# Optimization experiments

Hardware: AMD Instinct MI355X
Metric: run time of the kernel (lower is better)

Reference implementation:

```python
import jax, jax.numpy as jnp
import numpy as np
import math

B, S, D, H = 4, 1024, 1024, 16
DK = D // H
WINDOW = 128
NEG = -100000.0


def setup_inputs() -> dict:
    key = jax.random.key(0)
    kx, kw1, kb1, kw2, kb2 = jax.random.split(key, 5)
    x = jax.random.normal(kx, (B, S, D), dtype=jnp.float32)
    # sliding-window band mask: True where |i-j| <= WINDOW
    i = jnp.arange(S)
    band = (jnp.abs(i[:, None] - i[None, :]) <= WINDOW)
    mask = jnp.broadcast_to(band, (B, S, S))
    # second structured mask: causal
    causal = (i[:, None] >= i[None, :])
    mask2 = jnp.broadcast_to(causal, (B, S, S))
    scale = 1.0 / math.sqrt(D)
    Wqkv = jax.random.normal(kw1, (D, 3 * D), dtype=jnp.float32) * scale
    bqkv = jax.random.normal(kb1, (3 * D,), dtype=jnp.float32) * 0.01
    Wo = jax.random.normal(kw2, (D, D), dtype=jnp.float32) * scale
    bo = jax.random.normal(kb2, (D,), dtype=jnp.float32) * 0.01
    return {"x": x, "mask": mask, "mask2": mask2, "Wqkv": Wqkv, "bqkv": bqkv, "Wo": Wo, "bo": bo}


def reference(x, mask, mask2, Wqkv, bqkv, Wo, bo):
    b, s, d = x.shape
    qkv = x @ Wqkv + bqkv                      # [b, s, 3d]
    q, k, v = jnp.split(qkv, 3, axis=-1)
    # [b, s, h, dk] -> [b, h, s, dk]
    q = q.reshape(b, s, H, DK).transpose(0, 2, 1, 3)
    k = k.reshape(b, s, H, DK).transpose(0, 2, 1, 3)
    v = v.reshape(b, s, H, DK).transpose(0, 2, 1, 3)
    scores = jnp.einsum('bhtd,bhsd->bhts', q, k) / math.sqrt(DK)
    scores = jnp.where(mask[:, None, :, :], scores, NEG)
    scores = jnp.where(mask2[:, None, :, :], scores, NEG)
    weights = jax.nn.softmax(scores, axis=-1)  # [b, h, t, s]
    context = jnp.einsum('bhts,bhsd->bhtd', weights, v)
    context = context.transpose(0, 2, 1, 3).reshape(b, s, d)
    context = context @ Wo + bo
    return (context, weights)
```

## Files before the change

kernel.cpp:

```cpp
#include <hip/hip_runtime.h>

typedef short bf16x8 __attribute__((ext_vector_type(8)));
typedef float floatx4 __attribute__((ext_vector_type(4)));

#define GLOBAL_AS __attribute__((address_space(1)))
#define LDS_AS __attribute__((address_space(3)))

__device__ __forceinline__ void gload_lds16(const ushort* g, ushort* l) {
  __builtin_amdgcn_global_load_lds((const GLOBAL_AS void*)g, (LDS_AS void*)l, 16, 0, 0);
}

__device__ __forceinline__ ushort f2bf(float x) {
  uint u = __float_as_uint(x);
  return (ushort)((u + 0x7fffu + ((u >> 16) & 1u)) >> 16);
}

__global__ __launch_bounds__(256) void k_f32_to_bf16(const float4* __restrict__ in,
                                                     ushort4* __restrict__ out, int n4) {
  int g = blockIdx.x * 256 + threadIdx.x;
  if (g < n4) {
    float4 v = in[g];
    ushort4 o;
    o.x = f2bf(v.x); o.y = f2bf(v.y); o.z = f2bf(v.z); o.w = f2bf(v.w);
    out[g] = o;
  }
}

__global__ __launch_bounds__(256) void k_transpose2(const float* __restrict__ W1,
                                                    ushort* __restrict__ O1,
                                                    const float* __restrict__ W2,
                                                    ushort* __restrict__ O2) {
  __shared__ float tile[32][33];
  int bx = blockIdx.x;
  const float* in; ushort* out; int N;
  if (bx < 96) { in = W1; out = O1; N = 3072; }
  else         { in = W2; out = O2; N = 1024; bx -= 96; }
  const int K = 1024;
  int n0 = bx * 32, k0 = blockIdx.y * 32;
  int tx = threadIdx.x & 31, ty = threadIdx.x >> 5;
  #pragma unroll
  for (int r = ty; r < 32; r += 8)
    tile[r][tx] = in[(size_t)(k0 + r) * N + n0 + tx];
  __syncthreads();
  #pragma unroll
  for (int r = ty; r < 32; r += 8)
    out[(size_t)(n0 + r) * K + k0 + tx] = f2bf(tile[tx][r]);
}

template <int OUT_BF16, int BN>
__global__ __launch_bounds__(256) void k_gemm_bt(const ushort* __restrict__ A,
                                                 const ushort* __restrict__ Bt,
                                                 const float* __restrict__ bias,
                                                 void* __restrict__ Cout,
                                                 int M, int N, int K) {
  constexpr int NI = BN / 32;
  constexpr int NB = BN / 64;
  __shared__ ushort As[128 * 32];
  __shared__ ushort Bs[BN * 32];
  const int t = threadIdx.x;
  const int m0 = blockIdx.y * 128, n0 = blockIdx.x * BN;
  const int w = t >> 6, l = t & 63;
  const int wm = (w & 1) * 64, wn = (w >> 1) * (BN / 2);
  const int lr = l & 15, q8 = (l >> 4) * 8;
  const int lrow = l >> 2, lcol = (l & 3) * 8;

  floatx4 acc[4][NI];
  #pragma unroll
  for (int i = 0; i < 4; ++i)
    #pragma unroll
    for (int j = 0; j < NI; ++j) acc[i][j] = (floatx4){0.f, 0.f, 0.f, 0.f};

  for (int k0 = 0; k0 < K; k0 += 32) {
    __syncthreads();
    #pragma unroll
    for (int i = 0; i < 2; ++i) {
      int r0 = (w * 2 + i) * 16;
      gload_lds16(A + (size_t)(m0 + r0 + lrow) * K + k0 + lcol, As + r0 * 32);
    }
    #pragma unroll
    for (int i = 0; i < NB; ++i) {
      int r0 = (w * NB + i) * 16;
      gload_lds16(Bt + (size_t)(n0 + r0 + lrow) * K + k0 + lcol, Bs + r0 * 32);
    }
    __syncthreads();
    bf16x8 af[4], bfr[NI];
    #pragma unroll
    for (int mi = 0; mi < 4; ++mi)
      af[mi] = *(const bf16x8*)(As + (wm + mi * 16 + lr) * 32 + q8);
    #pragma unroll
    for (int ni = 0; ni < NI; ++ni)
      bfr[ni] = *(const bf16x8*)(Bs + (wn + ni * 16 + lr) * 32 + q8);
    #pragma unroll
    for (int mi = 0; mi < 4; ++mi)
      #pragma unroll
      for (int ni = 0; ni < NI; ++ni)
        acc[mi][ni] = __builtin_amdgcn_mfma_f32_16x16x32_bf16(af[mi], bfr[ni], acc[mi][ni], 0, 0, 0);
  }

  const int rq = (l >> 4) * 4;
  #pragma unroll
  for (int ni = 0; ni < NI; ++ni) {
    int col = n0 + wn + ni * 16 + lr;
    float bv = bias[col];
    #pragma unroll
    for (int mi = 0; mi < 4; ++mi) {
      int row = m0 + wm + mi * 16 + rq;
      #pragma unroll
      for (int r2 = 0; r2 < 4; ++r2) {
        float v = acc[mi][ni][r2] + bv;
        size_t idx = (size_t)(row + r2) * N + col;
        if (OUT_BF16) ((ushort*)Cout)[idx] = f2bf(v);
        else          ((float*)Cout)[idx] = v;
      }
    }
  }
}

__global__ __launch_bounds__(256) void k_attn(const ushort* __restrict__ qkv,
                                              float* __restrict__ wout,
                                              ushort* __restrict__ ctxout) {
  __shared__ ushort smKP[192 * 68];
  __shared__ ushort smVT[64 * 202];
  __shared__ ushort smQ[64 * 68];

  const int t = threadIdx.x;
  const int w = t >> 6, l = t & 63;
  const int lr = l & 15, q8 = (l >> 4) * 8, q4 = (l >> 4) * 4;
  const int iblk = blockIdx.x & 15;
  const int h = (blockIdx.x >> 4) & 15;
  const int b = blockIdx.x >> 8;
  const int i0 = iblk * 64;
  const int jb0 = i0 - 128;
  const int tok0 = b * 1024 + i0;
  const int qoff = h * 64, koff = 1024 + h * 64, voff = 2048 + h * 64;
  const size_t wbase = ((size_t)(b * 16 + h) * 1024 + i0) * 1024;

  {
    int jstart = jb0 < 0 ? 0 : jb0;
    int jend = i0 + 64;
    float4 z = {0.f, 0.f, 0.f, 0.f};
    for (int g = t; g < 64 * 256; g += 256) {
      int r = g >> 8, j = (g & 255) * 4;
      if (j < jstart || j >= jend)
        *(float4*)(wout + wbase + (size_t)r * 1024 + j) = z;
    }
  }

  #pragma unroll
  for (int c = 0; c < 2; ++c) {
    int idx = t + 256 * c, row = idx >> 3, ch = idx & 7;
    *(uint4*)(smQ + row * 68 + ch * 8) =
        *(const uint4*)(qkv + (size_t)(tok0 + row) * 3072 + qoff + ch * 8);
  }
  #pragma unroll
  for (int c = 0; c < 6; ++c) {
    int idx = t + 256 * c, row = idx >> 3, ch = idx & 7;
    int jsrc = jb0 + row; if (jsrc < 0) jsrc = 0;
    *(uint4*)(smKP + row * 68 + ch * 8) =
        *(const uint4*)(qkv + (size_t)(b * 1024 + jsrc) * 3072 + koff + ch * 8);
  }
  #pragma unroll
  for (int c = 0; c < 6; ++c) {
    int idx = t + 256 * c;
    int j = (idx & 15) + 16 * (idx >> 7);
    int d0 = ((idx >> 4) & 7) * 8;
    int jsrc = jb0 + j; if (jsrc < 0) jsrc = 0;
    uint4 u = *(const uint4*)(qkv + (size_t)(b * 1024 + jsrc) * 3072 + voff + d0);
    ushort* p = smVT + j;
    p[(d0 + 0) * 202] = (ushort)(u.x & 0xffffu);
    p[(d0 + 1) * 202] = (ushort)(u.x >> 16);
    p[(d0 + 2) * 202] = (ushort)(u.y & 0xffffu);
    p[(d0 + 3) * 202] = (ushort)(u.y >> 16);
    p[(d0 + 4) * 202] = (ushort)(u.z & 0xffffu);
    p[(d0 + 5) * 202] = (ushort)(u.z >> 16);
    p[(d0 + 6) * 202] = (ushort)(u.w & 0xffffu);
    p[(d0 + 7) * 202] = (ushort)(u.w >> 16);
  }
  __syncthreads();

  floatx4 sc[12];
  #pragma unroll
  for (int ni = 0; ni < 12; ++ni) sc[ni] = (floatx4){0.f, 0.f, 0.f, 0.f};
  bf16x8 aq0 = *(const bf16x8*)(smQ + (w * 16 + lr) * 68 + q8);
  bf16x8 aq1 = *(const bf16x8*)(smQ + (w * 16 + lr) * 68 + 32 + q8);
  #pragma unroll
  for (int ni = 0; ni < 12; ++ni) {
    bf16x8 bk0 = *(const bf16x8*)(smKP + (ni * 16 + lr) * 68 + q8);
    bf16x8 bk1 = *(const bf16x8*)(smKP + (ni * 16 + lr) * 68 + 32 + q8);
    sc[ni] = __builtin_amdgcn_mfma_f32_16x16x32_bf16(aq0, bk0, sc[ni], 0, 0, 0);
    sc[ni] = __builtin_amdgcn_mfma_f32_16x16x32_bf16(aq1, bk1, sc[ni], 0, 0, 0);
  }
  __syncthreads();

  float mrow[4] = {-3e38f, -3e38f, -3e38f, -3e38f};
  #pragma unroll
  for (int ni = 0; ni < 12; ++ni) {
    int nj = ni * 16 + lr;
    #pragma unroll
    for (int reg = 0; reg < 4; ++reg) {
      int di = w * 16 + q4 + reg;
      bool valid = (nj >= di) & (nj <= di + 128) & (jb0 + nj >= 0);
      float s = valid ? sc[ni][reg] * 0.125f : -3e38f;
      sc[ni][reg] = s;
      mrow[reg] = fmaxf(mrow[reg], s);
    }
  }
  #pragma unroll
  for (int reg = 0; reg < 4; ++reg) {
    #pragma unroll
    for (int off = 1; off < 16; off <<= 1)
      mrow[reg] = fmaxf(mrow[reg], __shfl_xor(mrow[reg], off, 64));
  }
  float lrow[4] = {0.f, 0.f, 0.f, 0.f};
  #pragma unroll
  for (int ni = 0; ni < 12; ++ni) {
    #pragma unroll
    for (int reg = 0; reg < 4; ++reg) {
      float e = __expf(sc[ni][reg] - mrow[reg]);
      sc[ni][reg] = e;
      lrow[reg] += e;
    }
  }
  float inv[4];
  #pragma unroll
  for (int reg = 0; reg < 4; ++reg) {
    float s = lrow[reg];
    #pragma unroll
    for (int off = 1; off < 16; off <<= 1) s += __shfl_xor(s, off, 64);
    inv[reg] = 1.0f / s;
  }

  ushort* smP = smKP;
  #pragma unroll
  for (int ni = 0; ni < 12; ++ni) {
    int nj = ni * 16 + lr;
    int j = jb0 + nj;
    #pragma unroll
    for (int reg = 0; reg < 4; ++reg) {
      int il = w * 16 + q4 + reg;
      float e = sc[ni][reg];
      if (j >= 0) wout[wbase + (size_t)il * 1024 + j] = e * inv[reg];
      smP[il * 202 + nj] = f2bf(e);
    }
  }

  floatx4 oc[4];
  #pragma unroll
  for (int ni = 0; ni < 4; ++ni) oc[ni] = (floatx4){0.f, 0.f, 0.f, 0.f};
  #pragma unroll
  for (int ks = 0; ks < 6; ++ks) {
    bf16x8 ap = *(const bf16x8*)(smP + (w * 16 + lr) * 202 + ks * 32 + q8);
    #pragma unroll
    for (int ni = 0; ni < 4; ++ni) {
      bf16x8 bv = *(const bf16x8*)(smVT + (ni * 16 + lr) * 202 + ks * 32 + q8);
      oc[ni] = __builtin_amdgcn_mfma_f32_16x16x32_bf16(ap, bv, oc[ni], 0, 0, 0);
    }
  }

  #pragma unroll
  for (int ni = 0; ni < 4; ++ni) {
    int d = ni * 16 + lr;
    #pragma unroll
    for (int reg = 0; reg < 4; ++reg) {
      int il = w * 16 + q4 + reg;
      ctxout[(size_t)(tok0 + il) * 1024 + qoff + d] = f2bf(oc[ni][reg] * inv[reg]);
    }
  }
}

extern "C" void kernel_launch(void* const* d_in, const int* in_sizes, int n_in,
                              void* d_out, int out_size, void* d_ws, size_t ws_size,
                              hipStream_t stream) {
  const float* x    = (const float*)d_in[0];
  const float* Wqkv = (const float*)d_in[3];
  const float* bqkv = (const float*)d_in[4];
  const float* Wo   = (const float*)d_in[5];
  const float* bo   = (const float*)d_in[6];

  float* out_ctx = (float*)d_out;
  float* out_w   = out_ctx + (size_t)4 * 1024 * 1024;

  char* ws = (char*)d_ws;
  ushort* qkv_bf = (ushort*)(ws);
  ushort* ctx_bf = (ushort*)(ws + 25165824);
  ushort* x_bf   = (ushort*)(ws + 33554432);
  ushort* WqkvT  = (ushort*)(ws + 41943040);
  ushort* WoT    = (ushort*)(ws + 48234496);

  k_f32_to_bf16<<<4096, 256, 0, stream>>>((const float4*)x, (ushort4*)x_bf, 1048576);
  k_transpose2<<<dim3(128, 32), 256, 0, stream>>>(Wqkv, WqkvT, Wo, WoT);
  k_gemm_bt<1, 128><<<dim3(24, 32), 256, 0, stream>>>(x_bf, WqkvT, bqkv, qkv_bf, 4096, 3072, 1024);
  k_attn<<<1024, 256, 0, stream>>>(qkv_bf, out_w, ctx_bf);
  k_gemm_bt<0, 64><<<dim3(16, 32), 256, 0, stream>>>(ctx_bf, WoT, bo, out_ctx, 4096, 1024, 1024);
}
```

Measured before the change: 407.5 us.

## Write attention weights in one coalesced full-row pass from LDS

The separate zero-fill pass and the scattered per-element weight stores are replaced by a final pass. After the PV matmul, each thread writes a float4 column slice of all 64 rows with nontemporal stores, reading the probabilities from the bf16 P tile in LDS and scaling by per-row inverse sums kept in shared memory. This aims to make the large weights write fully coalesced and to write each output byte only once. Q is now loaded straight from global memory into registers instead of being staged in LDS, and the LDS strides are adjusted. The trade-off is that the weights output now comes from bf16-rounded exponentials rather than fp32 values, which lowers its accuracy.

```diff
diff --git a/kernel.cpp b/kernel.cpp
--- a/kernel.cpp
+++ b/kernel.cpp
@@ -120,8 +120,8 @@
                                               float* __restrict__ wout,
                                               ushort* __restrict__ ctxout) {
   __shared__ ushort smKP[192 * 68];
-  __shared__ ushort smVT[64 * 202];
-  __shared__ ushort smQ[64 * 68];
+  __shared__ ushort smVT[64 * 200];
+  __shared__ float smInv[64];
 
   const int t = threadIdx.x;
   const int w = t >> 6, l = t & 63;
@@ -135,23 +135,6 @@
   const int qoff = h * 64, koff = 1024 + h * 64, voff = 2048 + h * 64;
   const size_t wbase = ((size_t)(b * 16 + h) * 1024 + i0) * 1024;
 
-  {
-    int jstart = jb0 < 0 ? 0 : jb0;
-    int jend = i0 + 64;
-    float4 z = {0.f, 0.f, 0.f, 0.f};
-    for (int g = t; g < 64 * 256; g += 256) {
-      int r = g >> 8, j = (g & 255) * 4;
-      if (j < jstart || j >= jend)
-        *(float4*)(wout + wbase + (size_t)r * 1024 + j) = z;
-    }
-  }
-
-  #pragma unroll
-  for (int c = 0; c < 2; ++c) {
-    int idx = t + 256 * c, row = idx >> 3, ch = idx & 7;
-    *(uint4*)(smQ + row * 68 + ch * 8) =
-        *(const uint4*)(qkv + (size_t)(tok0 + row) * 3072 + qoff + ch * 8);
-  }
   #pragma unroll
   for (int c = 0; c < 6; ++c) {
     int idx = t + 256 * c, row = idx >> 3, ch = idx & 7;
@@ -167,22 +150,24 @@
     int jsrc = jb0 + j; if (jsrc < 0) jsrc = 0;
     uint4 u = *(const uint4*)(qkv + (size_t)(b * 1024 + jsrc) * 3072 + voff + d0);
     ushort* p = smVT + j;
-    p[(d0 + 0) * 202] = (ushort)(u.x & 0xffffu);
-    p[(d0 + 1) * 202] = (ushort)(u.x >> 16);
-    p[(d0 + 2) * 202] = (ushort)(u.y & 0xffffu);
-    p[(d0 + 3) * 202] = (ushort)(u.y >> 16);
-    p[(d0 + 4) * 202] = (ushort)(u.z & 0xffffu);
-    p[(d0 + 5) * 202] = (ushort)(u.z >> 16);
-    p[(d0 + 6) * 202] = (ushort)(u.w & 0xffffu);
-    p[(d0 + 7) * 202] = (ushort)(u.w >> 16);
-  }
+    p[(d0 + 0) * 200] = (ushort)(u.x & 0xffffu);
+    p[(d0 + 1) * 200] = (ushort)(u.x >> 16);
+    p[(d0 + 2) * 200] = (ushort)(u.y & 0xffffu);
+    p[(d0 + 3) * 200] = (ushort)(u.y >> 16);
+    p[(d0 + 4) * 200] = (ushort)(u.z & 0xffffu);
+    p[(d0 + 5) * 200] = (ushort)(u.z >> 16);
+    p[(d0 + 6) * 200] = (ushort)(u.w & 0xffffu);
+    p[(d0 + 7) * 200] = (ushort)(u.w >> 16);
+  }
+
+  const ushort* qrow = qkv + (size_t)(tok0 + w * 16 + lr) * 3072 + qoff;
+  bf16x8 aq0 = *(const bf16x8*)(qrow + q8);
+  bf16x8 aq1 = *(const bf16x8*)(qrow + 32 + q8);
   __syncthreads();
 
   floatx4 sc[12];
   #pragma unroll
   for (int ni = 0; ni < 12; ++ni) sc[ni] = (floatx4){0.f, 0.f, 0.f, 0.f};
-  bf16x8 aq0 = *(const bf16x8*)(smQ + (w * 16 + lr) * 68 + q8);
-  bf16x8 aq1 = *(const bf16x8*)(smQ + (w * 16 + lr) * 68 + 32 + q8);
   #pragma unroll
   for (int ni = 0; ni < 12; ++ni) {
     bf16x8 bk0 = *(const bf16x8*)(smKP + (ni * 16 + lr) * 68 + q8);
@@ -234,14 +219,15 @@
   #pragma unroll
   for (int ni = 0; ni < 12; ++ni) {
     int nj = ni * 16 + lr;
-    int j = jb0 + nj;
     #pragma unroll
     for (int reg = 0; reg < 4; ++reg) {
       int il = w * 16 + q4 + reg;
-      float e = sc[ni][reg];
-      if (j >= 0) wout[wbase + (size_t)il * 1024 + j] = e * inv[reg];
-      smP[il * 202 + nj] = f2bf(e);
-    }
+      smP[il * 204 + nj] = f2bf(sc[ni][reg]);
+    }
+  }
+  if (lr == 0) {
+    #pragma unroll
+    for (int reg = 0; reg < 4; ++reg) smInv[w * 16 + q4 + reg] = inv[reg];
   }
 
   floatx4 oc[4];
@@ -249,10 +235,10 @@
   for (int ni = 0; ni < 4; ++ni) oc[ni] = (floatx4){0.f, 0.f, 0.f, 0.f};
   #pragma unroll
   for (int ks = 0; ks < 6; ++ks) {
-    bf16x8 ap = *(const bf16x8*)(smP + (w * 16 + lr) * 202 + ks * 32 + q8);
+    bf16x8 ap = *(const bf16x8*)(smP + (w * 16 + lr) * 204 + ks * 32 + q8);
     #pragma unroll
     for (int ni = 0; ni < 4; ++ni) {
-      bf16x8 bv = *(const bf16x8*)(smVT + (ni * 16 + lr) * 202 + ks * 32 + q8);
+      bf16x8 bv = *(const bf16x8*)(smVT + (ni * 16 + lr) * 200 + ks * 32 + q8);
       oc[ni] = __builtin_amdgcn_mfma_f32_16x16x32_bf16(ap, bv, oc[ni], 0, 0, 0);
     }
   }
@@ -264,6 +250,28 @@
     for (int reg = 0; reg < 4; ++reg) {
       int il = w * 16 + q4 + reg;
       ctxout[(size_t)(tok0 + il) * 1024 + qoff + d] = f2bf(oc[ni][reg] * inv[reg]);
+    }
+  }
+
+  __syncthreads();
+
+  {
+    const int j4 = t * 4;
+    const unsigned nj4 = (unsigned)(j4 - jb0);
+    const bool inband = nj4 < 192u;
+    const int njc = inband ? (int)nj4 : 0;
+    const float bandf = inband ? 1.0f : 0.0f;
+    float* wp = wout + wbase + j4;
+    const ushort* pp = smP + njc;
+    #pragma unroll 4
+    for (int r = 0; r < 64; ++r) {
+      ushort4 pv = *(const ushort4*)(pp + r * 204);
+      float iv = smInv[r] * bandf;
+      floatx4 o = { __uint_as_float((uint)pv.x << 16) * iv,
+                    __uint_as_float((uint)pv.y << 16) * iv,
+                    __uint_as_float((uint)pv.z << 16) * iv,
+                    __uint_as_float((uint)pv.w << 16) * iv };
+      __builtin_nontemporal_store(o, (floatx4*)(wp + (size_t)r * 1024));
     }
   }
 }
```

After: 399.3 us. 1.02x faster.
